# Kernel tuning notes

Measured on AMD Instinct MI355X. Metric: run time of the kernel, lower is better.

The kernel has to match this reference:

```python
import jax, jax.numpy as jnp
import numpy as np

D_MODEL = 1024
N_HEADS = 16
N_GROUPS = 4
CONTEXT_LEN = 512
D_H = D_MODEL // N_HEADS          # 64
GROUP_SIZE = N_HEADS // N_GROUPS  # 4
B, S = 4, 2048


def setup_inputs() -> dict:
    key = jax.random.key(0)
    ks = jax.random.split(key, 9)
    s = 0.02
    return {
        "x": jax.random.normal(ks[0], (B, S, D_MODEL), dtype=jnp.float32),
        "Wq": jax.random.normal(ks[1], (D_MODEL, D_MODEL), dtype=jnp.float32) * s,
        "bq": jax.random.normal(ks[2], (D_MODEL,), dtype=jnp.float32) * s,
        "Wk": jax.random.normal(ks[3], (D_MODEL, N_GROUPS * D_H), dtype=jnp.float32) * s,
        "bk": jax.random.normal(ks[4], (N_GROUPS * D_H,), dtype=jnp.float32) * s,
        "Wv": jax.random.normal(ks[5], (D_MODEL, N_GROUPS * D_H), dtype=jnp.float32) * s,
        "bv": jax.random.normal(ks[6], (N_GROUPS * D_H,), dtype=jnp.float32) * s,
        "Wo": jax.random.normal(ks[7], (D_MODEL, D_MODEL), dtype=jnp.float32) * s,
        "bo": jax.random.normal(ks[8], (D_MODEL,), dtype=jnp.float32) * s,
    }


def reference(x, Wq, bq, Wk, bk, Wv, bv, Wo, bo):
    b, s = x.shape[0], x.shape[1]
    # Projections. q: [b, n_groups, group_size, s, d_h]; k/v: [b, n_groups, s, d_h]
    q = (x @ Wq + bq).reshape(b, s, N_GROUPS, GROUP_SIZE, D_H)
    q = jnp.transpose(q, (0, 2, 3, 1, 4))
    k = jnp.transpose((x @ Wk + bk).reshape(b, s, N_GROUPS, D_H), (0, 2, 1, 3))
    v = jnp.transpose((x @ Wv + bv).reshape(b, s, N_GROUPS, D_H), (0, 2, 1, 3))
    # Grouped scores (einsum broadcast == repeat_interleave of k over group_size)
    scores = jnp.einsum("bghqd,bgkd->bghqk", q, k) / jnp.sqrt(jnp.float32(D_H))
    # Sliding-window causal mask (cached_len == s when use_cache=False)
    i = jnp.arange(s)
    j = jnp.arange(s)
    upper = (i - CONTEXT_LEN)[:, None] >= j[None, :]   # too-old keys
    lower = i[:, None] < j[None, :]                    # future keys
    mask = upper | lower                               # [s, s]
    scores = jnp.where(mask, jnp.float32(-1e9), scores)
    att = jax.nn.softmax(scores, axis=-1)
    out = jnp.einsum("bghqk,bgkd->bghqd", att, v)      # [b, g, h, s, d_h]
    out = jnp.transpose(out, (0, 3, 1, 2, 4)).reshape(b, s, D_MODEL)
    return out @ Wo + bo
```

## Files before the change

kernel.cpp:

```cpp
#include <hip/hip_runtime.h>
#include <cstdint>
#include <cstddef>

typedef __attribute__((ext_vector_type(8))) short short8;
typedef __attribute__((ext_vector_type(4))) short short4v;
typedef __attribute__((ext_vector_type(4))) float f32x4;
typedef __attribute__((ext_vector_type(4))) unsigned short ushort4v;
typedef unsigned short ushort_t;

union Frag8 { short4v h[2]; short8 v; };
union PFrag { unsigned int w[4]; short8 v; };

__device__ __forceinline__ ushort_t f2bf(float f) {
  unsigned int u = __builtin_bit_cast(unsigned int, f);
  u += 0x7FFFu + ((u >> 16) & 1u);
  return (ushort_t)(u >> 16);
}

__device__ __forceinline__ void gload16(const void* g, void* l) {
  __builtin_amdgcn_global_load_lds(
      (const __attribute__((address_space(1))) unsigned int*)g,
      (__attribute__((address_space(3))) unsigned int*)l, 16, 0, 0);
}

__global__ void cast_x_kernel(const float* __restrict__ x, ushort_t* __restrict__ o) {
  int i = (blockIdx.x * 256 + threadIdx.x) * 4;
  const float4 v = *reinterpret_cast<const float4*>(x + i);
  ushort4v r = { f2bf(v.x), f2bf(v.y), f2bf(v.z), f2bf(v.w) };
  *reinterpret_cast<ushort4v*>(o + i) = r;
}

__global__ __launch_bounds__(256) void transpose_w_kernel(
    const float* __restrict__ Wq, const float* __restrict__ Wk,
    const float* __restrict__ Wv, const float* __restrict__ Wo,
    ushort_t* __restrict__ Wt) {
  __shared__ float tile[32][33];
  const int tn = blockIdx.x, tk = blockIdx.y;
  const int n0 = tn * 32;
  const float* W; int ldn, nloc;
  if      (n0 < 1024) { W = Wq; ldn = 1024; nloc = n0; }
  else if (n0 < 1280) { W = Wk; ldn = 256;  nloc = n0 - 1024; }
  else if (n0 < 1536) { W = Wv; ldn = 256;  nloc = n0 - 1280; }
  else                { W = Wo; ldn = 1024; nloc = n0 - 1536; }
  const int t = threadIdx.x;
  const int sr = t >> 3, sc = (t & 7) * 4;
  const float4 v = *reinterpret_cast<const float4*>(W + (size_t)(tk * 32 + sr) * ldn + nloc + sc);
  tile[sr][sc] = v.x; tile[sr][sc + 1] = v.y; tile[sr][sc + 2] = v.z; tile[sr][sc + 3] = v.w;
  __syncthreads();
  const int wr = t >> 3, wc = (t & 7) * 4;
  ushort4v o = { f2bf(tile[wc][wr]), f2bf(tile[wc + 1][wr]),
                 f2bf(tile[wc + 2][wr]), f2bf(tile[wc + 3][wr]) };
  *reinterpret_cast<ushort4v*>(Wt + (size_t)(n0 + wr) * 1024 + tk * 32 + wc) = o;
}

__global__ void prep_bias_kernel(const float* __restrict__ bq, const float* __restrict__ bk,
                                 const float* __restrict__ bv, float* __restrict__ bqkv) {
  int t = blockIdx.x * 256 + threadIdx.x;
  if (t < 1536) bqkv[t] = (t < 1024) ? bq[t] : (t < 1280) ? bk[t - 1024] : bv[t - 1280];
}

#define GEMM_IDS \
  const int tid = threadIdx.x;                        \
  const int w = tid >> 6, lane = tid & 63;            \
  const int wm = w >> 1, wn = w & 1;                  \
  const int g = lane >> 4, r16 = lane & 15;           \
  const int l8 = lane & 7, lr = lane >> 3;

#define GEMM_KLOOP(APTR, BPTR, KBYTES, NT)                                              \
  const f32x4 vzero = {0.f, 0.f, 0.f, 0.f};                                             \
  f32x4 acc[4][4];                                                                      \
  _Pragma("unroll") for (int i = 0; i < 4; ++i)                                         \
    _Pragma("unroll") for (int j = 0; j < 4; ++j) acc[i][j] = vzero;                    \
  auto stage = [&](int buf, int k0) {                                                   \
    _Pragma("unroll") for (int i = 0; i < 4; ++i) {                                     \
      const int c = w * 4 + i;                                                          \
      const int row = c * 8 + lr;                                                       \
      const int u = l8 ^ (row & 7);                                                     \
      gload16((const char*)(APTR) + (size_t)(bm * 128 + row) * (KBYTES) + k0 * 2 + u * 16, \
              AsB + buf * 16384 + c * 1024);                                            \
      gload16((const char*)(BPTR) + (size_t)(bn * 128 + row) * (KBYTES) + k0 * 2 + u * 16, \
              BsB + buf * 16384 + c * 1024);                                            \
    }                                                                                   \
  };                                                                                    \
  stage(0, 0);                                                                          \
  __syncthreads();                                                                      \
  for (int t = 0; t < (NT); ++t) {                                                      \
    const int cur = t & 1;                                                              \
    if (t + 1 < (NT)) stage(cur ^ 1, (t + 1) * 64);                                     \
    const char* Ac = AsB + cur * 16384;                                                 \
    const char* Bc = BsB + cur * 16384;                                                 \
    _Pragma("unroll") for (int kc = 0; kc < 2; ++kc) {                                  \
      short8 af[4], bf[4];                                                              \
      _Pragma("unroll") for (int mi = 0; mi < 4; ++mi) {                                \
        const int row = wm * 64 + mi * 16 + r16;                                        \
        af[mi] = *(const short8*)(Ac + row * 128 + ((((kc << 2) | g) ^ (r16 & 7)) << 4)); \
      }                                                                                 \
      _Pragma("unroll") for (int ni = 0; ni < 4; ++ni) {                                \
        const int row = wn * 64 + ni * 16 + r16;                                        \
        bf[ni] = *(const short8*)(Bc + row * 128 + ((((kc << 2) | g) ^ (r16 & 7)) << 4)); \
      }                                                                                 \
      _Pragma("unroll") for (int mi = 0; mi < 4; ++mi)                                  \
        _Pragma("unroll") for (int ni = 0; ni < 4; ++ni)                                \
          acc[mi][ni] = __builtin_amdgcn_mfma_f32_16x16x32_bf16(af[mi], bf[ni], acc[mi][ni], 0, 0, 0); \
    }                                                                                   \
    __syncthreads();                                                                    \
  }

__global__ __launch_bounds__(256, 2) void gemm_qkv_kernel(
    const ushort_t* __restrict__ A, const ushort_t* __restrict__ Bt,
    const float* __restrict__ bias,
    ushort_t* __restrict__ Qb, ushort_t* __restrict__ Kb, ushort_t* __restrict__ Vt)
{
  __shared__ __align__(16) char AsB[32768];
  __shared__ __align__(16) char BsB[32768];
  const int xcd = blockIdx.x & 7, ii = blockIdx.x >> 3;
  const int bm = xcd * 8 + (ii & 7), bn = ii >> 3;
  GEMM_IDS
  GEMM_KLOOP(A, Bt, 2048, 16)

  float bcol[4];
#pragma unroll
  for (int ni = 0; ni < 4; ++ni) bcol[ni] = bias[bn * 128 + wn * 64 + ni * 16 + r16];
  const int bb = bm >> 4;
  if (bn < 8) {
#pragma unroll
    for (int mi = 0; mi < 4; ++mi)
#pragma unroll
      for (int ni = 0; ni < 4; ++ni) {
        const int col = bn * 128 + wn * 64 + ni * 16 + r16;
#pragma unroll
        for (int rr = 0; rr < 4; ++rr) {
          const int row = bm * 128 + wm * 64 + mi * 16 + g * 4 + rr;
          Qb[(size_t)row * 1024 + col] = f2bf(acc[mi][ni][rr] + bcol[ni]);
        }
      }
  } else if (bn < 10) {
#pragma unroll
    for (int mi = 0; mi < 4; ++mi)
#pragma unroll
      for (int ni = 0; ni < 4; ++ni) {
        const int c = bn * 128 + wn * 64 + ni * 16 + r16 - 1024;
        const int gi = c >> 6, dd = c & 63;
#pragma unroll
        for (int rr = 0; rr < 4; ++rr) {
          const int row = bm * 128 + wm * 64 + mi * 16 + g * 4 + rr;
          const int s = row & 2047;
          Kb[((size_t)(bb * 4 + gi) * 2048 + s) * 64 + dd] = f2bf(acc[mi][ni][rr] + bcol[ni]);
        }
      }
  } else {
#pragma unroll
    for (int mi = 0; mi < 4; ++mi) {
      const int s0 = (bm * 128 + wm * 64 + mi * 16 + g * 4) & 2047;
#pragma unroll
      for (int ni = 0; ni < 4; ++ni) {
        const int c = bn * 128 + wn * 64 + ni * 16 + r16 - 1280;
        const int gi = c >> 6, dd = c & 63;
        ushort4v pk;
#pragma unroll
        for (int rr = 0; rr < 4; ++rr) pk[rr] = f2bf(acc[mi][ni][rr] + bcol[ni]);
        *reinterpret_cast<ushort4v*>(Vt + ((size_t)(bb * 4 + gi) * 64 + dd) * 2048 + s0) = pk;
      }
    }
  }
}

__global__ __launch_bounds__(256, 2) void gemm_out_kernel(
    const ushort_t* __restrict__ A, const ushort_t* __restrict__ Bt,
    const float* __restrict__ bias, float* __restrict__ Cout)
{
  __shared__ __align__(16) char AsB[32768];
  __shared__ __align__(16) char BsB[32768];
  const int xcd = blockIdx.x & 7, ii = blockIdx.x >> 3;
  const int bm = xcd * 8 + (ii & 7), bn = ii >> 3;
  GEMM_IDS
  GEMM_KLOOP(A, Bt, 2048, 16)

  float bcol[4];
#pragma unroll
  for (int ni = 0; ni < 4; ++ni) bcol[ni] = bias[bn * 128 + wn * 64 + ni * 16 + r16];
#pragma unroll
  for (int mi = 0; mi < 4; ++mi)
#pragma unroll
    for (int ni = 0; ni < 4; ++ni) {
      const int col = bn * 128 + wn * 64 + ni * 16 + r16;
#pragma unroll
      for (int rr = 0; rr < 4; ++rr) {
        const int row = bm * 128 + wm * 64 + mi * 16 + g * 4 + rr;
        Cout[(size_t)row * 1024 + col] = acc[mi][ni][rr] + bcol[ni];
      }
    }
}

__global__ __launch_bounds__(512, 2) void attn_kernel(
    const ushort_t* __restrict__ Qb, const ushort_t* __restrict__ Kb,
    const ushort_t* __restrict__ Vt, ushort_t* __restrict__ attout)
{
  __shared__ __align__(16) char KsB[16384];
  __shared__ __align__(16) char VsB[16384];
  const int fid = blockIdx.x + 32 * (blockIdx.y + 4 * blockIdx.z);
  const int j = fid >> 3;
  const int qt = (fid & 7) * 4 + (j >> 4);
  const int gg = j & 3, b = (j >> 2) & 3;

  const int tid = threadIdx.x;
  const int w = tid >> 6, lane = tid & 63;
  const int hw = w & 3, qh = w >> 2;
  const int h = gg * 4 + hw;
  const int g = lane >> 4, r16 = lane & 15;
  const int u0 = g >> 1;
  const int lowb = (g & 1) << 3;
  const int q0w = qt * 64 + qh * 32;

  short8 qf[2][2];
#pragma unroll
  for (int qs = 0; qs < 2; ++qs) {
    const char* qptr = (const char*)Qb + ((size_t)(b * 2048 + q0w + qs * 16 + r16) * 1024 + h * 64) * 2;
#pragma unroll
    for (int dc = 0; dc < 2; ++dc)
      qf[qs][dc] = *(const short8*)(qptr + dc * 64 + g * 16);
  }

  const f32x4 vzero = {0.f, 0.f, 0.f, 0.f};
  f32x4 accO[2][4];
#pragma unroll
  for (int qs = 0; qs < 2; ++qs)
#pragma unroll
    for (int nt = 0; nt < 4; ++nt) accO[qs][nt] = vzero;
  float lsum[2] = {0.f, 0.f};

  const char* KbB = (const char*)Kb + (size_t)(b * 4 + gg) * 2048 * 128;
  const char* VtB = (const char*)Vt + (size_t)(b * 4 + gg) * 64 * 4096;

  const int kb0 = (qt >= 8) ? (qt * 64 - 512) : 0;
  const int NT = (qt * 64 + 64 - kb0) >> 6;

  const int srr = tid >> 3, spk = tid & 7;
  auto stage = [&](int buf, int kb) {
    gload16(KbB + (size_t)(kb + srr) * 128 + ((spk ^ (srr & 7)) << 4),
            KsB + buf * 8192 + tid * 16);
    gload16(VtB + (size_t)srr * 4096 + (size_t)kb * 2 + ((spk ^ (srr & 7)) << 4),
            VsB + buf * 8192 + tid * 16);
  };

  stage(0, kb0);
  __syncthreads();
  for (int t = 0; t < NT; ++t) {
    const int kb = kb0 + t * 64;
    const int cur = t & 1;
    if (t + 1 < NT) stage(cur ^ 1, kb + 64);
    const char* Ks = KsB + cur * 8192;
    const char* Vs = VsB + cur * 8192;
    const bool full = (kb >= q0w - 480) && (kb <= q0w - 63);

    f32x4 st[2][4];
#pragma unroll
    for (int ki = 0; ki < 4; ++ki) {
      const int key = ki * 16 + r16;
      const int swz = key & 7;
      const short8 kf0 = *(const short8*)(Ks + key * 128 + ((g ^ swz) << 4));
      const short8 kf1 = *(const short8*)(Ks + key * 128 + (((4 + g) ^ swz) << 4));
#pragma unroll
      for (int qs = 0; qs < 2; ++qs) {
        st[qs][ki] = __builtin_amdgcn_mfma_f32_16x16x32_bf16(kf0, qf[qs][0], vzero, 0, 0, 0);
        st[qs][ki] = __builtin_amdgcn_mfma_f32_16x16x32_bf16(kf1, qf[qs][1], st[qs][ki], 0, 0, 0);
      }
    }

    PFrag pf[2][2];
#pragma unroll
    for (int qs = 0; qs < 2; ++qs) {
      const int q = q0w + qs * 16 + r16;
#pragma unroll
      for (int ki = 0; ki < 4; ++ki)
#pragma unroll
        for (int r = 0; r < 4; ++r) {
          float s = st[qs][ki][r] * 0.180336881f;
          if (!full) {
            const int key = kb + ki * 16 + g * 4 + r;
            const bool valid = (key <= q) && (key + 512 > q);
            s = valid ? s : -INFINITY;
          }
          st[qs][ki][r] = __builtin_amdgcn_exp2f(s);
        }
      float tk[4];
#pragma unroll
      for (int ki = 0; ki < 4; ++ki)
        tk[ki] = (st[qs][ki][0] + st[qs][ki][1]) + (st[qs][ki][2] + st[qs][ki][3]);
      lsum[qs] += (tk[0] + tk[1]) + (tk[2] + tk[3]);
#pragma unroll
      for (int c = 0; c < 2; ++c)
#pragma unroll
        for (int pr = 0; pr < 2; ++pr) {
          asm("v_cvt_pk_bf16_f32 %0, %1, %2"
              : "=v"(pf[qs][c].w[pr * 2])
              : "v"(st[qs][2 * c + pr][0]), "v"(st[qs][2 * c + pr][1]));
          asm("v_cvt_pk_bf16_f32 %0, %1, %2"
              : "=v"(pf[qs][c].w[pr * 2 + 1])
              : "v"(st[qs][2 * c + pr][2]), "v"(st[qs][2 * c + pr][3]));
        }
    }

#pragma unroll
    for (int c = 0; c < 2; ++c)
#pragma unroll
      for (int nt = 0; nt < 4; ++nt) {
        const int d = nt * 16 + r16;
        const int swz = d & 7;
        Frag8 vf;
        vf.h[0] = *(const short4v*)(Vs + d * 128 + (((c * 4 + u0) ^ swz) << 4) + lowb);
        vf.h[1] = *(const short4v*)(Vs + d * 128 + (((c * 4 + 2 + u0) ^ swz) << 4) + lowb);
#pragma unroll
        for (int qs = 0; qs < 2; ++qs)
          accO[qs][nt] = __builtin_amdgcn_mfma_f32_16x16x32_bf16(pf[qs][c].v, vf.v, accO[qs][nt], 0, 0, 0);
      }
    __syncthreads();
  }

#pragma unroll
  for (int qs = 0; qs < 2; ++qs) {
    float ts = lsum[qs];
    ts += __shfl_xor(ts, 16);
    ts += __shfl_xor(ts, 32);
    const float linv = 1.f / ts;
    float lq[4];
#pragma unroll
    for (int rr = 0; rr < 4; ++rr) lq[rr] = __shfl(linv, g * 4 + rr);
#pragma unroll
    for (int nt = 0; nt < 4; ++nt) {
      const int ocol = h * 64 + nt * 16 + r16;
#pragma unroll
      for (int rr = 0; rr < 4; ++rr) {
        const int orow = b * 2048 + q0w + qs * 16 + g * 4 + rr;
        attout[(size_t)orow * 1024 + ocol] = f2bf(accO[qs][nt][rr] * lq[rr]);
      }
    }
  }
}

extern "C" void kernel_launch(void* const* d_in, const int* in_sizes, int n_in,
                              void* d_out, int out_size, void* d_ws, size_t ws_size,
                              hipStream_t stream) {
  (void)in_sizes; (void)n_in; (void)out_size; (void)ws_size;
  const float* x  = (const float*)d_in[0];
  const float* Wq = (const float*)d_in[1];
  const float* bq = (const float*)d_in[2];
  const float* Wk = (const float*)d_in[3];
  const float* bk = (const float*)d_in[4];
  const float* Wv = (const float*)d_in[5];
  const float* bv = (const float*)d_in[6];
  const float* Wo = (const float*)d_in[7];
  const float* bo = (const float*)d_in[8];

  char* ws = (char*)d_ws;
  ushort_t* Qb   = (ushort_t*)(ws + 0);
  ushort_t* Kb   = (ushort_t*)(ws + 16777216);
  ushort_t* Vt   = (ushort_t*)(ws + 20971520);
  ushort_t* wt   = (ushort_t*)(ws + 25165824);
  float*    bqkv = (float*)   (ws + 30408704);
  ushort_t* xb   = (ushort_t*)(ws + 30416896);
  ushort_t* att  = (ushort_t*)(ws + 47194112);

  cast_x_kernel<<<8192, 256, 0, stream>>>(x, xb);
  transpose_w_kernel<<<dim3(80, 32), 256, 0, stream>>>(Wq, Wk, Wv, Wo, wt);
  prep_bias_kernel<<<6, 256, 0, stream>>>(bq, bk, bv, bqkv);
  gemm_qkv_kernel<<<768, 256, 0, stream>>>(xb, wt, bqkv, Qb, Kb, Vt);
  attn_kernel<<<dim3(32, 4, 4), 512, 0, stream>>>(Qb, Kb, Vt, att);
  gemm_out_kernel<<<512, 256, 0, stream>>>(att, wt + (size_t)1536 * 1024, bo, (float*)d_out);
}
```

Measured before the change: 120.8 us.

## Use 256x128 GEMM tiles with triple-buffered K=32 LDS pipeline

Both projection GEMMs move from 128x128 to 256x128 block tiles, with each wave computing 128x64. The K-loop now takes 32-wide slices through a three-stage LDS ring with explicit vmcnt waits and raw barriers, uses a new XOR swizzle, and raises wave priority around the MFMA burst. The aim is more operand reuse per LDS load and deeper prefetch that hides global latency. The cost is half as many blocks (384 and 256), which may underfill the CUs, plus 72KB of LDS per block that likely allows only one or two blocks per CU, and higher register pressure from 32 accumulators.

```diff
diff --git a/kernel.cpp b/kernel.cpp
--- a/kernel.cpp
+++ b/kernel.cpp
@@ -63,47 +63,48 @@
   const int tid = threadIdx.x;                        \
   const int w = tid >> 6, lane = tid & 63;            \
   const int wm = w >> 1, wn = w & 1;                  \
-  const int g = lane >> 4, r16 = lane & 15;           \
-  const int l8 = lane & 7, lr = lane >> 3;
-
-#define GEMM_KLOOP(APTR, BPTR, KBYTES, NT)                                              \
+  const int g = lane >> 4, r16 = lane & 15;
+
+#define GEMM_KLOOP(APTR, BPTR)                                                          \
   const f32x4 vzero = {0.f, 0.f, 0.f, 0.f};                                             \
-  f32x4 acc[4][4];                                                                      \
-  _Pragma("unroll") for (int i = 0; i < 4; ++i)                                         \
+  f32x4 acc[8][4];                                                                      \
+  _Pragma("unroll") for (int i = 0; i < 8; ++i)                                         \
     _Pragma("unroll") for (int j = 0; j < 4; ++j) acc[i][j] = vzero;                    \
-  auto stage = [&](int buf, int k0) {                                                   \
+  const int su = (lane & 3) ^ ((lane >> 3) & 3);                                        \
+  const int sr = lane >> 2;                                                             \
+  auto stage = [&](int s, int k0) {                                                     \
+    char* base = LdsB + s * 24576;                                                      \
     _Pragma("unroll") for (int i = 0; i < 4; ++i) {                                     \
       const int c = w * 4 + i;                                                          \
-      const int row = c * 8 + lr;                                                       \
-      const int u = l8 ^ (row & 7);                                                     \
-      gload16((const char*)(APTR) + (size_t)(bm * 128 + row) * (KBYTES) + k0 * 2 + u * 16, \
-              AsB + buf * 16384 + c * 1024);                                            \
-      gload16((const char*)(BPTR) + (size_t)(bn * 128 + row) * (KBYTES) + k0 * 2 + u * 16, \
-              BsB + buf * 16384 + c * 1024);                                            \
+      gload16((const char*)(APTR) + (size_t)(bm * 256 + c * 16 + sr) * 2048 + k0 * 2 + su * 16, \
+              base + c * 1024);                                                         \
+    }                                                                                   \
+    _Pragma("unroll") for (int i = 0; i < 2; ++i) {                                     \
+      const int c = w * 2 + i;                                                          \
+      gload16((const char*)(BPTR) + (size_t)(bn * 128 + c * 16 + sr) * 2048 + k0 * 2 + su * 16, \
+              base + 16384 + c * 1024);                                                 \
     }                                                                                   \
   };                                                                                    \
   stage(0, 0);                                                                          \
-  __syncthreads();                                                                      \
-  for (int t = 0; t < (NT); ++t) {                                                      \
-    const int cur = t & 1;                                                              \
-    if (t + 1 < (NT)) stage(cur ^ 1, (t + 1) * 64);                                     \
-    const char* Ac = AsB + cur * 16384;                                                 \
-    const char* Bc = BsB + cur * 16384;                                                 \
-    _Pragma("unroll") for (int kc = 0; kc < 2; ++kc) {                                  \
-      short8 af[4], bf[4];                                                              \
-      _Pragma("unroll") for (int mi = 0; mi < 4; ++mi) {                                \
-        const int row = wm * 64 + mi * 16 + r16;                                        \
-        af[mi] = *(const short8*)(Ac + row * 128 + ((((kc << 2) | g) ^ (r16 & 7)) << 4)); \
-      }                                                                                 \
-      _Pragma("unroll") for (int ni = 0; ni < 4; ++ni) {                                \
-        const int row = wn * 64 + ni * 16 + r16;                                        \
-        bf[ni] = *(const short8*)(Bc + row * 128 + ((((kc << 2) | g) ^ (r16 & 7)) << 4)); \
-      }                                                                                 \
-      _Pragma("unroll") for (int mi = 0; mi < 4; ++mi)                                  \
-        _Pragma("unroll") for (int ni = 0; ni < 4; ++ni)                                \
-          acc[mi][ni] = __builtin_amdgcn_mfma_f32_16x16x32_bf16(af[mi], bf[ni], acc[mi][ni], 0, 0, 0); \
-    }                                                                                   \
-    __syncthreads();                                                                    \
+  stage(1, 32);                                                                         \
+  const int fsw = (g ^ ((r16 >> 1) & 3)) << 4;                                          \
+  for (int t = 0; t < 32; ++t) {                                                        \
+    if (t < 31) { asm volatile("s_waitcnt vmcnt(6) lgkmcnt(0)" ::: "memory"); }         \
+    else        { asm volatile("s_waitcnt vmcnt(0) lgkmcnt(0)" ::: "memory"); }         \
+    __builtin_amdgcn_s_barrier();                                                       \
+    if (t + 2 < 32) stage((t + 2) % 3, (t + 2) * 32);                                   \
+    const char* Ab = LdsB + (t % 3) * 24576;                                            \
+    const char* Bb = Ab + 16384;                                                        \
+    short8 af[8], bf[4];                                                                \
+    _Pragma("unroll") for (int mi = 0; mi < 8; ++mi)                                    \
+      af[mi] = *(const short8*)(Ab + (wm * 128 + mi * 16 + r16) * 64 + fsw);            \
+    _Pragma("unroll") for (int ni = 0; ni < 4; ++ni)                                    \
+      bf[ni] = *(const short8*)(Bb + (wn * 64 + ni * 16 + r16) * 64 + fsw);             \
+    __builtin_amdgcn_s_setprio(1);                                                      \
+    _Pragma("unroll") for (int mi = 0; mi < 8; ++mi)                                    \
+      _Pragma("unroll") for (int ni = 0; ni < 4; ++ni)                                  \
+        acc[mi][ni] = __builtin_amdgcn_mfma_f32_16x16x32_bf16(af[mi], bf[ni], acc[mi][ni], 0, 0, 0); \
+    __builtin_amdgcn_s_setprio(0);                                                      \
   }
 
 __global__ __launch_bounds__(256, 2) void gemm_qkv_kernel(
@@ -111,47 +112,46 @@
     const float* __restrict__ bias,
     ushort_t* __restrict__ Qb, ushort_t* __restrict__ Kb, ushort_t* __restrict__ Vt)
 {
-  __shared__ __align__(16) char AsB[32768];
-  __shared__ __align__(16) char BsB[32768];
+  __shared__ __align__(16) char LdsB[73728];
   const int xcd = blockIdx.x & 7, ii = blockIdx.x >> 3;
-  const int bm = xcd * 8 + (ii & 7), bn = ii >> 3;
+  const int bm = xcd * 4 + ii / 12, bn = ii % 12;
   GEMM_IDS
-  GEMM_KLOOP(A, Bt, 2048, 16)
+  GEMM_KLOOP(A, Bt)
 
   float bcol[4];
 #pragma unroll
   for (int ni = 0; ni < 4; ++ni) bcol[ni] = bias[bn * 128 + wn * 64 + ni * 16 + r16];
-  const int bb = bm >> 4;
   if (bn < 8) {
 #pragma unroll
-    for (int mi = 0; mi < 4; ++mi)
+    for (int mi = 0; mi < 8; ++mi)
 #pragma unroll
       for (int ni = 0; ni < 4; ++ni) {
         const int col = bn * 128 + wn * 64 + ni * 16 + r16;
 #pragma unroll
         for (int rr = 0; rr < 4; ++rr) {
-          const int row = bm * 128 + wm * 64 + mi * 16 + g * 4 + rr;
+          const int row = bm * 256 + wm * 128 + mi * 16 + g * 4 + rr;
           Qb[(size_t)row * 1024 + col] = f2bf(acc[mi][ni][rr] + bcol[ni]);
         }
       }
   } else if (bn < 10) {
 #pragma unroll
-    for (int mi = 0; mi < 4; ++mi)
+    for (int mi = 0; mi < 8; ++mi)
 #pragma unroll
       for (int ni = 0; ni < 4; ++ni) {
         const int c = bn * 128 + wn * 64 + ni * 16 + r16 - 1024;
         const int gi = c >> 6, dd = c & 63;
 #pragma unroll
         for (int rr = 0; rr < 4; ++rr) {
-          const int row = bm * 128 + wm * 64 + mi * 16 + g * 4 + rr;
-          const int s = row & 2047;
+          const int row = bm * 256 + wm * 128 + mi * 16 + g * 4 + rr;
+          const int bb = row >> 11, s = row & 2047;
           Kb[((size_t)(bb * 4 + gi) * 2048 + s) * 64 + dd] = f2bf(acc[mi][ni][rr] + bcol[ni]);
         }
       }
   } else {
 #pragma unroll
-    for (int mi = 0; mi < 4; ++mi) {
-      const int s0 = (bm * 128 + wm * 64 + mi * 16 + g * 4) & 2047;
+    for (int mi = 0; mi < 8; ++mi) {
+      const int row0 = bm * 256 + wm * 128 + mi * 16 + g * 4;
+      const int bb = row0 >> 11, s0 = row0 & 2047;
 #pragma unroll
       for (int ni = 0; ni < 4; ++ni) {
         const int c = bn * 128 + wn * 64 + ni * 16 + r16 - 1280;
@@ -169,24 +169,23 @@
     const ushort_t* __restrict__ A, const ushort_t* __restrict__ Bt,
     const float* __restrict__ bias, float* __restrict__ Cout)
 {
-  __shared__ __align__(16) char AsB[32768];
-  __shared__ __align__(16) char BsB[32768];
+  __shared__ __align__(16) char LdsB[73728];
   const int xcd = blockIdx.x & 7, ii = blockIdx.x >> 3;
-  const int bm = xcd * 8 + (ii & 7), bn = ii >> 3;
+  const int bm = xcd * 4 + (ii >> 3), bn = ii & 7;
   GEMM_IDS
-  GEMM_KLOOP(A, Bt, 2048, 16)
+  GEMM_KLOOP(A, Bt)
 
   float bcol[4];
 #pragma unroll
   for (int ni = 0; ni < 4; ++ni) bcol[ni] = bias[bn * 128 + wn * 64 + ni * 16 + r16];
 #pragma unroll
-  for (int mi = 0; mi < 4; ++mi)
+  for (int mi = 0; mi < 8; ++mi)
 #pragma unroll
     for (int ni = 0; ni < 4; ++ni) {
       const int col = bn * 128 + wn * 64 + ni * 16 + r16;
 #pragma unroll
       for (int rr = 0; rr < 4; ++rr) {
-        const int row = bm * 128 + wm * 64 + mi * 16 + g * 4 + rr;
+        const int row = bm * 256 + wm * 128 + mi * 16 + g * 4 + rr;
         Cout[(size_t)row * 1024 + col] = acc[mi][ni][rr] + bcol[ni];
       }
     }
@@ -364,7 +363,7 @@
   cast_x_kernel<<<8192, 256, 0, stream>>>(x, xb);
   transpose_w_kernel<<<dim3(80, 32), 256, 0, stream>>>(Wq, Wk, Wv, Wo, wt);
   prep_bias_kernel<<<6, 256, 0, stream>>>(bq, bk, bv, bqkv);
-  gemm_qkv_kernel<<<768, 256, 0, stream>>>(xb, wt, bqkv, Qb, Kb, Vt);
+  gemm_qkv_kernel<<<384, 256, 0, stream>>>(xb, wt, bqkv, Qb, Kb, Vt);
   attn_kernel<<<dim3(32, 4, 4), 512, 0, stream>>>(Qb, Kb, Vt, att);
-  gemm_out_kernel<<<512, 256, 0, stream>>>(att, wt + (size_t)1536 * 1024, bo, (float*)d_out);
-}
+  gemm_out_kernel<<<256, 256, 0, stream>>>(att, wt + (size_t)1536 * 1024, bo, (float*)d_out);
+}
```

Result: no change. 118.7 us (-1.7%).
